# Kernel tuning notes

Hardware: AMD Instinct MI355X
Metric: run time of the kernel (lower is better)

The kernel has to match this reference:

```python
import jax, jax.numpy as jnp
import numpy as np

N, E, B = 20000, 320000, 64
NODE_DIM, EDGE_DIM, H, T = 64, 32, 128, 256
L = 5            # propagation_depth
DELTA = 1.0      # avg_d['log']
N_AGG, N_SCAL = 4, 3


def _w(k, shape):
    return jax.random.normal(k, shape, jnp.float32) / np.sqrt(shape[-2])


def setup_inputs() -> dict:
    key = jax.random.key(0)
    ks = jax.random.split(key, 12)
    return {
        "node_feat": jax.random.normal(ks[0], (N, NODE_DIM), jnp.float32),
        "edge_feat": jax.random.normal(ks[1], (E, EDGE_DIM), jnp.float32),
        "W_in": _w(ks[2], (NODE_DIM, H)),
        "b_in": jnp.zeros((H,), jnp.float32),
        "pre_W": _w(ks[3], (L, 2 * H + EDGE_DIM, H)),
        "pre_b": jnp.zeros((L, H), jnp.float32),
        "post_W": _w(ks[4], (L, H + N_AGG * N_SCAL * H, H)),
        "post_b": jnp.zeros((L, H), jnp.float32),
        "out_W1": _w(ks[5], (3 * H, H)),
        "out_b1": jnp.zeros((H,), jnp.float32),
        "out_W2": _w(ks[6], (H, T)),
        "out_b2": jnp.zeros((T,), jnp.float32),
        "src": jax.random.randint(ks[7], (E,), 0, N),
        "dst": jax.random.randint(ks[8], (E,), 0, N),
        "node2graph": jnp.sort(jax.random.randint(ks[9], (N,), 0, B)),
    }


def _forward(node_feat, edge_feat, W_in, b_in, pre_W, pre_b, post_W, post_b,
             out_W1, out_b1, out_W2, out_b2, src, dst, node2graph):
    # input node MLP (Linear + ReLU)
    h = jax.nn.relu(node_feat @ W_in + b_in)                       # [N, H]

    # degree-based scalers (constant across layers)
    deg = jax.ops.segment_sum(jnp.ones((E,), h.dtype), dst, num_segments=N)
    has_edge = (deg > 0)[:, None]
    inv_deg = jnp.where(deg > 0, 1.0 / jnp.maximum(deg, 1.0), 0.0)[:, None]
    logd = jnp.log(deg + 1.0)
    amp = (logd / DELTA)[:, None]                                  # amplification
    att = jnp.where(logd > 0, DELTA / jnp.maximum(logd, 1e-12), 1.0)[:, None]

    def step(h, p):
        pW, pb, qW, qb = p
        # pretrans on concat(src feat, dst feat, edge feat)
        m_in = jnp.concatenate([h[src], h[dst], edge_feat], axis=-1)  # [E, 2H+De]
        m = jax.nn.relu(m_in @ pW + pb)                               # [E, H]
        # multi-aggregator gather
        s = jax.ops.segment_sum(m, dst, num_segments=N)
        mean = s * inv_deg
        mx = jnp.where(has_edge, jax.ops.segment_max(m, dst, num_segments=N), 0.0)
        mn = jnp.where(has_edge, jax.ops.segment_min(m, dst, num_segments=N), 0.0)
        agg = jnp.concatenate([mean, mx, mn, s], axis=-1)             # [N, 4H]
        scaled = jnp.concatenate([agg, agg * amp, agg * att], axis=-1)  # [N, 12H]
        # posttrans on concat(h, aggregated)
        h_new = jax.nn.relu(jnp.concatenate([h, scaled], axis=-1) @ qW + qb)
        return h + h_new, None                                        # residual

    h, _ = jax.lax.scan(step, h, (pre_W, pre_b, post_W, post_b))

    # multi-aggregator readout over graphs
    g_sum = jax.ops.segment_sum(h, node2graph, num_segments=B)
    g_cnt = jax.ops.segment_sum(jnp.ones((N, 1), h.dtype), node2graph, num_segments=B)
    g_mean = g_sum / jnp.maximum(g_cnt, 1.0)
    g_max = jnp.where(g_cnt > 0, jax.ops.segment_max(h, node2graph, num_segments=B), 0.0)
    readout = jnp.concatenate([g_mean, g_max, g_sum], axis=-1)        # [B, 3H]
    return jax.nn.relu(readout @ out_W1 + out_b1) @ out_W2 + out_b2   # [B, T]


def reference(node_feat, edge_feat, W_in, b_in, pre_W, pre_b, post_W, post_b,
              out_W1, out_b1, out_W2, out_b2, src, dst, node2graph):
    return _forward(node_feat, edge_feat, W_in, b_in, pre_W, pre_b, post_W, post_b,
                    out_W1, out_b1, out_W2, out_b2, src, dst, node2graph)
```

## Files before the change

### kernel.cpp

```cpp
#include <hip/hip_runtime.h>

#define H 128
#define NODE_DIM 64
#define EDGE_DIM 32
#define KPRE (2*H + EDGE_DIM)
#define KPOST (13*H)
#define T_OUT 256
#define L_DEPTH 5
#define POST_FRAGS (52*8*64)
#define Y_FRAGS (4*16*64)
#define EF_FRAGS (8*64)
#define RCH 8

typedef short short8v __attribute__((ext_vector_type(8)));
typedef float float4v __attribute__((ext_vector_type(4)));

__device__ __forceinline__ unsigned short f2bf(float x) {
    unsigned int b = __float_as_uint(x);
    return (unsigned short)((b + 0x7fffu + ((b >> 16) & 1u)) >> 16);
}
__device__ __forceinline__ float bf2f(unsigned short u) {
    return __uint_as_float((unsigned int)u << 16);
}

__global__ void k_input_mlp(const float* __restrict__ nf, const float* __restrict__ W,
                            const float* __restrict__ b, float* __restrict__ h,
                            unsigned short* __restrict__ h_bf, int N) {
    int gid = blockIdx.x * blockDim.x + threadIdx.x;
    int n = gid >> 7, c = gid & 127;
    if (n >= N) return;
    const float* nrow = nf + (size_t)n * NODE_DIM;
    float acc = 0.f;
#pragma unroll 8
    for (int k = 0; k < NODE_DIM; ++k)
        acc += nrow[k] * W[k * H + c];
    acc += b[c];
    acc = fmaxf(acc, 0.f);
    h[(size_t)n * H + c] = acc;
    h_bf[(size_t)n * H + c] = f2bf(acc);
}

__global__ void k_hist(const int* __restrict__ dst, int* __restrict__ deg_i, int E) {
    int e = blockIdx.x * blockDim.x + threadIdx.x;
    if (e < E) atomicAdd(&deg_i[dst[e]], 1);
}

__global__ __launch_bounds__(1024) void k_scan(const int* __restrict__ deg_i,
                                               int* __restrict__ row_start,
                                               int* __restrict__ cursor, int N) {
    __shared__ int part[1024];
    int t = threadIdx.x;
    int per = (N + 1023) / 1024;
    int base = t * per;
    int s = 0;
    for (int i = 0; i < per; ++i) {
        int idx = base + i;
        if (idx < N) s += deg_i[idx];
    }
    part[t] = s;
    __syncthreads();
    for (int off = 1; off < 1024; off <<= 1) {
        int v = (t >= off) ? part[t - off] : 0;
        __syncthreads();
        part[t] += v;
        __syncthreads();
    }
    int run = (t == 0) ? 0 : part[t - 1];
    for (int i = 0; i < per; ++i) {
        int idx = base + i;
        if (idx < N) {
            row_start[idx] = run;
            cursor[idx] = run;
            run += deg_i[idx];
        }
    }
    if (t == 1023) row_start[N] = run;
}

__global__ void k_sortscatter(const int* __restrict__ src, const int* __restrict__ dst,
                              int* __restrict__ cursor, int* __restrict__ es_src,
                              int* __restrict__ es_eid, int E) {
    int e = blockIdx.x * blockDim.x + threadIdx.x;
    if (e >= E) return;
    int pos = atomicAdd(&cursor[dst[e]], 1);
    es_src[pos] = src[e];
    es_eid[pos] = e;
}

__global__ void k_efsort(const float* __restrict__ ef, const int* __restrict__ es_eid,
                         unsigned short* __restrict__ efs_bf, int E) {
    int t = blockIdx.x * 256 + threadIdx.x;
    int p = t >> 2, q = t & 3;
    if (p >= E) return;
    int eid = es_eid[p];
    const float* sp = ef + (size_t)eid * EDGE_DIM + q * 8;
    float4 v0 = *(const float4*)sp;
    float4 v1 = *(const float4*)(sp + 4);
    short8v o;
    o[0] = (short)f2bf(v0.x); o[1] = (short)f2bf(v0.y);
    o[2] = (short)f2bf(v0.z); o[3] = (short)f2bf(v0.w);
    o[4] = (short)f2bf(v1.x); o[5] = (short)f2bf(v1.y);
    o[6] = (short)f2bf(v1.z); o[7] = (short)f2bf(v1.w);
    *(short8v*)(efs_bf + (size_t)p * EDGE_DIM + q * 8) = o;
}

__global__ void k_scalers(const int* __restrict__ deg_i, float* __restrict__ invd,
                          float* __restrict__ amp, float* __restrict__ att, int N) {
    int n = blockIdx.x * blockDim.x + threadIdx.x;
    if (n >= N) return;
    float d = (float)deg_i[n];
    invd[n] = (d > 0.f) ? (1.f / d) : 0.f;
    float ld = logf(d + 1.f);
    amp[n] = ld;
    att[n] = (d > 0.f) ? (1.f / ld) : 1.f;
}

__global__ void k_gbounds(const int* __restrict__ n2g, int* __restrict__ g_start,
                          int N, int B) {
    int n = blockIdx.x * 256 + threadIdx.x;
    if (n > N) return;
    int cur = (n < N) ? n2g[n] : B;
    int prev = (n == 0) ? -1 : n2g[n - 1];
    for (int g = prev + 1; g <= cur && g <= B; ++g)
        g_start[g] = n;
}

__global__ void k_wconv_all(const float* __restrict__ pre_W,
                            const float* __restrict__ post_W,
                            short* __restrict__ wf_y_all,
                            short* __restrict__ wf_post_all,
                            short* __restrict__ wf_ef_all) {
    const int wrow[13] = {0, 256, 384, 512, 768, 896, 1024, 1280, 1408, 1536, 128, 640, 1152};
    int t = blockIdx.x * 256 + threadIdx.x;
    if (t < L_DEPTH * POST_FRAGS) {
        int l = t / POST_FRAGS, tt = t - l * POST_FRAGS;
        const float* qW = post_W + (size_t)l * KPOST * H;
        int lane = tt & 63, fc = tt >> 6;
        int b = fc >> 5, ks = (fc >> 3) & 3, cb = fc & 7;
        int col = cb * 16 + (lane & 15);
        int k0 = wrow[b] + ks * 32 + ((lane >> 4) << 3);
        short8v o;
#pragma unroll
        for (int j = 0; j < 8; ++j)
            o[j] = (short)f2bf(qW[(size_t)(k0 + j) * H + col]);
        *(short8v*)(wf_post_all + (size_t)t * 8) = o;
        return;
    }
    t -= L_DEPTH * POST_FRAGS;
    if (t < L_DEPTH * Y_FRAGS) {
        int l = t / Y_FRAGS, tt = t - l * Y_FRAGS;
        const float* pW = pre_W + (size_t)l * KPRE * H;
        int lane = tt & 63, fc = tt >> 6;
        int kglob = fc >> 4, cb = fc & 15;
        int col = cb * 16 + (lane & 15);
        int k0 = kglob * 32 + ((lane >> 4) << 3);
        int rowoff = (col < 128) ? 0 : 128;
        int c = col & 127;
        short8v o;
#pragma unroll
        for (int j = 0; j < 8; ++j)
            o[j] = (short)f2bf(pW[(size_t)(rowoff + k0 + j) * H + c]);
        *(short8v*)(wf_y_all + (size_t)t * 8) = o;
        return;
    }
    t -= L_DEPTH * Y_FRAGS;
    if (t >= L_DEPTH * EF_FRAGS) return;
    int l = t / EF_FRAGS, tt = t - l * EF_FRAGS;
    int lane = tt & 63, cb = tt >> 6;
    int col = cb * 16 + (lane & 15);
    int k0 = (lane >> 4) << 3;
    const float* pW = pre_W + (size_t)l * KPRE * H;
    short8v o;
#pragma unroll
    for (int j = 0; j < 8; ++j)
        o[j] = (short)f2bf(pW[(size_t)(2 * H + k0 + j) * H + col]);
    *(short8v*)(wf_ef_all + (size_t)t * 8) = o;
}

__global__ __launch_bounds__(256) void k_ygemm_mfma(
    const unsigned short* __restrict__ h_bf, const short* __restrict__ Wf,
    unsigned short* __restrict__ Y1bf, unsigned short* __restrict__ Y2bf, int N)
{
    __shared__ __align__(16) short Xs[64 * 128];
    int tid = threadIdx.x;
    int n0 = blockIdx.x * 64;
    int lane = tid & 63, wave = tid >> 6;
    float4v acc[16];
#pragma unroll
    for (int cb = 0; cb < 16; ++cb) acc[cb] = (float4v){0.f, 0.f, 0.f, 0.f};

    int rs = tid >> 4, c0 = (tid & 15) * 8;
#pragma unroll
    for (int j = 0; j < 4; ++j) {
        int r = rs + j * 16;
        int n = n0 + r;
        uint4 v = make_uint4(0, 0, 0, 0);
        if (n < N) v = *(const uint4*)(h_bf + (size_t)n * H + c0);
        *(uint4*)((char*)Xs + r * 256 + ((c0 * 2) ^ ((r & 7) << 4))) = v;
    }
    __syncthreads();
    int rloc = wave * 16 + (lane & 15);
    int swz = (rloc & 7) << 4;
#pragma unroll
    for (int ks = 0; ks < 4; ++ks) {
        int boff = rloc * 256 + (((ks * 64) + ((lane >> 4) << 4)) ^ swz);
        short8v a = *(short8v*)((char*)Xs + boff);
        const short* wp = Wf + ((size_t)(ks * 16) * 64 + lane) * 8;
#pragma unroll
        for (int cb = 0; cb < 16; ++cb) {
            short8v b = *(const short8v*)(wp + (size_t)cb * 512);
            acc[cb] = __builtin_amdgcn_mfma_f32_16x16x32_bf16(a, b, acc[cb], 0, 0, 0);
        }
    }
    int col0 = lane & 15;
    int row0 = wave * 16 + ((lane >> 4) << 2);
#pragma unroll
    for (int cb = 0; cb < 16; ++cb) {
        int col = cb * 16 + col0;
#pragma unroll
        for (int r = 0; r < 4; ++r) {
            int n = n0 + row0 + r;
            if (n < N) {
                if (col < 128) Y1bf[(size_t)n * H + col] = f2bf(acc[cb][r]);
                else           Y2bf[(size_t)n * H + (col - 128)] = f2bf(acc[cb][r]);
            }
        }
    }
}

__global__ __launch_bounds__(256) void k_efw(
    const unsigned short* __restrict__ efs_bf, const short* __restrict__ WfEf,
    unsigned short* __restrict__ EFW, int E)
{
    __shared__ __align__(16) unsigned short buf[4][16][128];
    int tid = threadIdx.x, lane = tid & 63, w = tid >> 6;
    int p0 = blockIdx.x * 256 + w * 64;
    short8v bfr[8];
#pragma unroll
    for (int cb = 0; cb < 8; ++cb)
        bfr[cb] = *(const short8v*)(WfEf + (size_t)(cb * 64 + lane) * 8);
#pragma unroll
    for (int t4 = 0; t4 < 4; ++t4) {
        int rowb = p0 + t4 * 16;
        int ar = rowb + (lane & 15);
        short8v a = {};
        if (ar < E)
            a = *(const short8v*)(efs_bf + (size_t)ar * EDGE_DIM + ((lane >> 4) << 3));
        float4v acc[8];
#pragma unroll
        for (int cb = 0; cb < 8; ++cb)
            acc[cb] = __builtin_amdgcn_mfma_f32_16x16x32_bf16(
                a, bfr[cb], (float4v){0.f, 0.f, 0.f, 0.f}, 0, 0, 0);
#pragma unroll
        for (int cb = 0; cb < 8; ++cb)
#pragma unroll
            for (int r = 0; r < 4; ++r)
                buf[w][((lane >> 4) << 2) + r][cb * 16 + (lane & 15)] = f2bf(acc[cb][r]);
#pragma unroll
        for (int j = 0; j < 4; ++j) {
            int lr = (lane >> 4) + j * 4;
            int gr = rowb + lr;
            uint4 v = *(const uint4*)&buf[w][lr][(lane & 15) * 8];
            if (gr < E)
                *(uint4*)(EFW + (size_t)gr * H + (lane & 15) * 8) = v;
        }
    }
}

__global__ __launch_bounds__(256) void k_edge_agg(
    const unsigned short* __restrict__ Y1bf, const unsigned short* __restrict__ Y2bf,
    const unsigned short* __restrict__ EFW, const float* __restrict__ pb,
    const int* __restrict__ es_src, const int* __restrict__ row_start,
    unsigned short* __restrict__ s_out, unsigned short* __restrict__ mx_out,
    unsigned short* __restrict__ mn_out, int N)
{
    __shared__ float red[4][3][128];
    int n = blockIdx.x;
    int tid = threadIdx.x, lane = tid & 63, w = tid >> 6;
    int start = row_start[n], end = row_start[n + 1];
    int cnt = end - start;
    int per = (cnt + 3) >> 2;
    int p0 = start + w * per;
    int p1 = min(p0 + per, end);
    unsigned int y2u = *(const unsigned int*)(Y2bf + (size_t)n * H + 2 * lane);
    float2 pbv = *(const float2*)(pb + 2 * lane);
    float y20 = bf2f((unsigned short)(y2u & 0xffffu)) + pbv.x;
    float y21 = bf2f((unsigned short)(y2u >> 16)) + pbv.y;
    float s0 = 0.f, s1 = 0.f;
    float mx0 = -3.4e38f, mx1 = -3.4e38f, mn0 = 3.4e38f, mn1 = 3.4e38f;
#pragma unroll 2
    for (int p = p0; p < p1; ++p) {
        int sn = __builtin_amdgcn_readfirstlane(es_src[p]);
        unsigned int y1u = *(const unsigned int*)(Y1bf + (size_t)sn * H + 2 * lane);
        unsigned int eu  = *(const unsigned int*)(EFW + (size_t)p * H + 2 * lane);
        float m0 = fmaxf(bf2f((unsigned short)(y1u & 0xffffu)) +
                         bf2f((unsigned short)(eu & 0xffffu)) + y20, 0.f);
        float m1 = fmaxf(bf2f((unsigned short)(y1u >> 16)) +
                         bf2f((unsigned short)(eu >> 16)) + y21, 0.f);
        s0 += m0; s1 += m1;
        mx0 = fmaxf(mx0, m0); mx1 = fmaxf(mx1, m1);
        mn0 = fminf(mn0, m0); mn1 = fminf(mn1, m1);
    }
    red[w][0][2 * lane] = s0;  red[w][0][2 * lane + 1] = s1;
    red[w][1][2 * lane] = mx0; red[w][1][2 * lane + 1] = mx1;
    red[w][2][2 * lane] = mn0; red[w][2][2 * lane + 1] = mn1;
    __syncthreads();
    if (tid < 128) {
        int c = tid;
        float s  = (red[0][0][c] + red[1][0][c]) + (red[2][0][c] + red[3][0][c]);
        float mx = fmaxf(fmaxf(red[0][1][c], red[1][1][c]),
                         fmaxf(red[2][1][c], red[3][1][c]));
        float mn = fminf(fminf(red[0][2][c], red[1][2][c]),
                         fminf(red[2][2][c], red[3][2][c]));
        if (cnt == 0) { s = 0.f; mx = 0.f; mn = 0.f; }
        size_t o = (size_t)n * H + c;
        s_out[o] = f2bf(s); mx_out[o] = f2bf(mx); mn_out[o] = f2bf(mn);
    }
}

__global__ __launch_bounds__(256) void k_post_mfma(
    float* __restrict__ h, unsigned short* __restrict__ h_bf,
    const unsigned short* __restrict__ s_in, const unsigned short* __restrict__ mx_in,
    const unsigned short* __restrict__ mn_in,
    const float* __restrict__ invd, const float* __restrict__ amp,
    const float* __restrict__ att,
    const short* __restrict__ Wf, const float* __restrict__ qb,
    const short* __restrict__ WfY, unsigned short* __restrict__ Y1bf,
    unsigned short* __restrict__ Y2bf, int doY, int N)
{
    __shared__ __align__(16) short Xs[32 * 128];
    int tid = threadIdx.x, lane = tid & 63, wave = tid >> 6;
    int rh = wave & 1, ch = wave >> 1;
    int n0 = blockIdx.x * 32;

    const unsigned short* const srcs[13] = {h_bf, mx_in, mn_in, s_in, mx_in, mn_in, s_in,
                                            mx_in, mn_in, s_in, s_in, s_in, s_in};
    const int grp_of[13] = {0, 0, 0, 0, 1, 1, 1, 2, 2, 2, 3, 4, 5};

    float4v acc[6][4];
#pragma unroll
    for (int g = 0; g < 6; ++g)
#pragma unroll
        for (int cb = 0; cb < 4; ++cb) acc[g][cb] = (float4v){0.f, 0.f, 0.f, 0.f};

    int arow = n0 + rh * 16 + (lane & 15);
    bool aok = arow < N;
    size_t abase = (size_t)arow * H + ((lane >> 4) << 3);

#pragma unroll
    for (int b = 0; b < 13; ++b) {
        const unsigned short* sp = srcs[b];
#pragma unroll
        for (int ks = 0; ks < 4; ++ks) {
            short8v a = {};
            if (aok) a = *(const short8v*)(sp + abase + ks * 32);
#pragma unroll
            for (int cb = 0; cb < 4; ++cb) {
                short8v bfrag = *(const short8v*)(
                    Wf + ((size_t)((b * 4 + ks) * 8 + ch * 4 + cb) * 64 + lane) * 8);
                acc[grp_of[b]][cb] =
                    __builtin_amdgcn_mfma_f32_16x16x32_bf16(a, bfrag, acc[grp_of[b]][cb], 0, 0, 0);
            }
        }
    }

    int col0 = lane & 15;
    int row0 = rh * 16 + ((lane >> 4) << 2);
    float s_invd[4], s_amp[4], s_att[4];
#pragma unroll
    for (int r = 0; r < 4; ++r) {
        int n = n0 + row0 + r;
        bool ok = n < N;
        s_invd[r] = ok ? invd[n] : 0.f;
        s_amp[r]  = ok ? amp[n]  : 0.f;
        s_att[r]  = ok ? att[n]  : 0.f;
    }
#pragma unroll
    for (int cb = 0; cb < 4; ++cb) {
        int col = (ch * 4 + cb) * 16 + col0;
        float bb = qb[col];
#pragma unroll
        for (int r = 0; r < 4; ++r) {
            int n = n0 + row0 + r;
            if (n < N) {
                float v = acc[0][cb][r]
                        + s_amp[r] * acc[1][cb][r] + s_att[r] * acc[2][cb][r]
                        + s_invd[r] * (acc[3][cb][r] + s_amp[r] * acc[4][cb][r]
                                       + s_att[r] * acc[5][cb][r]);
                size_t o = (size_t)n * H + col;
                float nv = h[o] + fmaxf(v + bb, 0.f);
                h[o] = nv;
                unsigned short us = f2bf(nv);
                h_bf[o] = us;
                if (doY) {
                    int rr = row0 + r;
                    *(short*)((char*)Xs + rr * 256 + ((col * 2) ^ ((rr & 7) << 4))) = (short)us;
                }
            }
        }
    }
    if (doY) {
        __syncthreads();
        float4v yacc[8];
#pragma unroll
        for (int i = 0; i < 8; ++i) yacc[i] = (float4v){0.f, 0.f, 0.f, 0.f};
#pragma unroll
        for (int t16 = 0; t16 < 2; ++t16) {
            int rloc = t16 * 16 + (lane & 15);
            int swz = (rloc & 7) << 4;
#pragma unroll
            for (int ks = 0; ks < 4; ++ks) {
                int boff = rloc * 256 + (((ks * 64) + ((lane >> 4) << 4)) ^ swz);
                short8v a = *(short8v*)((char*)Xs + boff);
#pragma unroll
                for (int cb = 0; cb < 4; ++cb) {
                    const short* wp = WfY + ((size_t)(ks * 16 + wave * 4 + cb) * 64 + lane) * 8;
                    short8v b = *(const short8v*)wp;
                    yacc[t16 * 4 + cb] =
                        __builtin_amdgcn_mfma_f32_16x16x32_bf16(a, b, yacc[t16 * 4 + cb], 0, 0, 0);
                }
            }
        }
#pragma unroll
        for (int t16 = 0; t16 < 2; ++t16) {
#pragma unroll
            for (int cb = 0; cb < 4; ++cb) {
                int col = (wave * 4 + cb) * 16 + col0;
                int r0 = t16 * 16 + ((lane >> 4) << 2);
#pragma unroll
                for (int r = 0; r < 4; ++r) {
                    int n = n0 + r0 + r;
                    if (n < N) {
                        unsigned short v = f2bf(yacc[t16 * 4 + cb][r]);
                        if (col < 128) Y1bf[(size_t)n * H + col] = v;
                        else           Y2bf[(size_t)n * H + (col - 128)] = v;
                    }
                }
            }
        }
    }
}

__global__ __launch_bounds__(256) void k_readout_part(
    const float* __restrict__ h, const int* __restrict__ g_start,
    float* __restrict__ psum, float* __restrict__ pmax, int B)
{
    __shared__ float rs[2][128], rm[2][128];
    int blk = blockIdx.x;
    int b = blk / RCH, chunk = blk % RCH;
    int tid = threadIdx.x;
    int c = tid & 127, half = tid >> 7;
    int g0 = g_start[b], g1 = g_start[b + 1];
    int cnt = g1 - g0;
    int per = (cnt + RCH - 1) / RCH;
    int n0 = g0 + chunk * per;
    int n1 = min(n0 + per, g1);
    float s = 0.f, m = -3.4e38f;
    for (int n = n0 + half; n < n1; n += 2) {
        float v = h[(size_t)n * H + c];
        s += v;
        m = fmaxf(m, v);
    }
    rs[half][c] = s;
    rm[half][c] = m;
    __syncthreads();
    if (tid < 128) {
        size_t o = ((size_t)b * RCH + chunk) * H + c;
        psum[o] = rs[0][c] + rs[1][c];
        pmax[o] = fmaxf(rm[0][c], rm[1][c]);
    }
}

__global__ __launch_bounds__(256) void k_readout_final2(
    const float* __restrict__ psum, const float* __restrict__ pmax,
    const int* __restrict__ g_start,
    const float* __restrict__ W1, const float* __restrict__ b1,
    const float* __restrict__ W2, const float* __restrict__ b2,
    float* __restrict__ out)
{
    __shared__ float xv[3 * H];
    __shared__ float hid[H];
    int b = blockIdx.x, tid = threadIdx.x;
    int cnt = g_start[b + 1] - g_start[b];
    if (tid < 128) {
        int c = tid;
        float s = 0.f, m = -3.4e38f;
#pragma unroll
        for (int j = 0; j < RCH; ++j) {
            size_t o = ((size_t)b * RCH + j) * H + c;
            s += psum[o];
            m = fmaxf(m, pmax[o]);
        }
        float rc = 1.f / fmaxf((float)cnt, 1.f);
        xv[c]         = s * rc;
        xv[H + c]     = (cnt > 0) ? m : 0.f;
        xv[2 * H + c] = s;
    }
    __syncthreads();
    if (tid < 128) {
        float acc = 0.f;
        for (int k = 0; k < 3 * H; ++k)
            acc += xv[k] * W1[k * H + tid];
        hid[tid] = fmaxf(acc + b1[tid], 0.f);
    }
    __syncthreads();
    float acc = 0.f;
#pragma unroll 8
    for (int k = 0; k < H; ++k)
        acc += hid[k] * W2[k * T_OUT + tid];
    out[(size_t)b * T_OUT + tid] = acc + b2[tid];
}

extern "C" void kernel_launch(void* const* d_in, const int* in_sizes, int n_in,
                              void* d_out, int out_size, void* d_ws, size_t ws_size,
                              hipStream_t stream) {
    const float* node_feat = (const float*)d_in[0];
    const float* edge_feat = (const float*)d_in[1];
    const float* W_in  = (const float*)d_in[2];
    const float* b_in  = (const float*)d_in[3];
    const float* pre_W = (const float*)d_in[4];
    const float* pre_b = (const float*)d_in[5];
    const float* post_W = (const float*)d_in[6];
    const float* post_b = (const float*)d_in[7];
    const float* out_W1 = (const float*)d_in[8];
    const float* out_b1 = (const float*)d_in[9];
    const float* out_W2 = (const float*)d_in[10];
    const float* out_b2 = (const float*)d_in[11];
    const int* src = (const int*)d_in[12];
    const int* dst = (const int*)d_in[13];
    const int* n2g = (const int*)d_in[14];

    int N = in_sizes[0] / NODE_DIM;
    int E = in_sizes[1] / EDGE_DIM;
    int B = out_size / T_OUT;
    float* out = (float*)d_out;

    float* ws = (float*)d_ws;
    float* h    = ws; ws += (size_t)N * H;
    float* invd = ws; ws += N;
    float* amp  = ws; ws += N;
    float* att  = ws; ws += N;
    float* psum = ws; ws += (size_t)B * RCH * H;
    float* pmax = ws; ws += (size_t)B * RCH * H;
    ws = (float*)(((uintptr_t)ws + 15) & ~(uintptr_t)15);
    unsigned short* h_bf  = (unsigned short*)ws;
    unsigned short* s_buf = h_bf  + (size_t)N * H;
    unsigned short* mx    = s_buf + (size_t)N * H;
    unsigned short* mn    = mx    + (size_t)N * H;
    unsigned short* Y1bf  = mn    + (size_t)N * H;
    unsigned short* Y2bf  = Y1bf  + (size_t)N * H;
    unsigned short* efs_bf = Y2bf + (size_t)N * H;
    unsigned short* EFW    = efs_bf + (size_t)E * EDGE_DIM;
    short* wf_post_all = (short*)(EFW + (size_t)E * H);
    short* wf_y_all    = wf_post_all + (size_t)L_DEPTH * POST_FRAGS * 8;
    short* wf_ef_all   = wf_y_all + (size_t)L_DEPTH * Y_FRAGS * 8;
    int* deg_i     = (int*)(wf_ef_all + (size_t)L_DEPTH * EF_FRAGS * 8);
    int* row_start = deg_i + N;
    int* cursor    = row_start + N + 1;
    int* es_src    = cursor + N;
    int* es_eid    = es_src + E;
    int* g_start   = es_eid + E;

    k_input_mlp<<<((size_t)N * H + 255) / 256, 256, 0, stream>>>(node_feat, W_in, b_in,
                                                                 h, h_bf, N);

    hipMemsetAsync(deg_i, 0, (size_t)N * sizeof(int), stream);
    k_hist<<<(E + 255) / 256, 256, 0, stream>>>(dst, deg_i, E);
    k_scan<<<1, 1024, 0, stream>>>(deg_i, row_start, cursor, N);
    k_sortscatter<<<(E + 255) / 256, 256, 0, stream>>>(src, dst, cursor, es_src, es_eid, E);
    k_efsort<<<((size_t)E * 4 + 255) / 256, 256, 0, stream>>>(edge_feat, es_eid, efs_bf, E);
    k_scalers<<<(N + 255) / 256, 256, 0, stream>>>(deg_i, invd, amp, att, N);
    k_gbounds<<<(N + 256) / 256, 256, 0, stream>>>(n2g, g_start, N, B);

    {
        int tot = L_DEPTH * (POST_FRAGS + Y_FRAGS + EF_FRAGS);
        k_wconv_all<<<(tot + 255) / 256, 256, 0, stream>>>(pre_W, post_W, wf_y_all,
                                                           wf_post_all, wf_ef_all);
    }

    k_ygemm_mfma<<<(N + 63) / 64, 256, 0, stream>>>(h_bf, wf_y_all, Y1bf, Y2bf, N);

    for (int l = 0; l < L_DEPTH; ++l) {
        k_efw<<<(E + 255) / 256, 256, 0, stream>>>(
            efs_bf, wf_ef_all + (size_t)l * EF_FRAGS * 8, EFW, E);
        k_edge_agg<<<N, 256, 0, stream>>>(
            Y1bf, Y2bf, EFW, pre_b + (size_t)l * H,
            es_src, row_start, s_buf, mx, mn, N);
        int doY = (l < L_DEPTH - 1) ? 1 : 0;
        k_post_mfma<<<(N + 31) / 32, 256, 0, stream>>>(
            h, h_bf, s_buf, mx, mn, invd, amp, att,
            wf_post_all + (size_t)l * POST_FRAGS * 8, post_b + (size_t)l * H,
            doY ? (wf_y_all + (size_t)(l + 1) * Y_FRAGS * 8) : wf_y_all,
            Y1bf, Y2bf, doY, N);
    }

    k_readout_part<<<B * RCH, 256, 0, stream>>>(h, g_start, psum, pmax, B);
    k_readout_final2<<<B, 256, 0, stream>>>(psum, pmax, g_start,
                                            out_W1, out_b1, out_W2, out_b2, out);
}
```

Baseline: 715.3 us.

## Map one wave per node in edge aggregation and halve post-MFMA row tile

The edge aggregation kernel now assigns one wavefront per destination node, four nodes per block, instead of splitting each node's edges across four waves. This removes the shared-memory reduction and block barrier, and writes outputs as packed 32-bit stores. The post-transform MFMA kernel now uses 16-row tiles with each wave owning 32 output columns, which doubles the block count to raise occupancy but re-reads the weight fragments more often. The per-node work is now serialized within one wave, so high-degree nodes take longer.

```diff
diff --git a/kernel.cpp b/kernel.cpp
--- a/kernel.cpp
+++ b/kernel.cpp
@@ -274,22 +274,20 @@
     unsigned short* __restrict__ s_out, unsigned short* __restrict__ mx_out,
     unsigned short* __restrict__ mn_out, int N)
 {
-    __shared__ float red[4][3][128];
-    int n = blockIdx.x;
     int tid = threadIdx.x, lane = tid & 63, w = tid >> 6;
+    int n = blockIdx.x * 4 + w;
+    if (n >= N) return;
     int start = row_start[n], end = row_start[n + 1];
-    int cnt = end - start;
-    int per = (cnt + 3) >> 2;
-    int p0 = start + w * per;
-    int p1 = min(p0 + per, end);
+    bool any = end > start;
     unsigned int y2u = *(const unsigned int*)(Y2bf + (size_t)n * H + 2 * lane);
     float2 pbv = *(const float2*)(pb + 2 * lane);
     float y20 = bf2f((unsigned short)(y2u & 0xffffu)) + pbv.x;
     float y21 = bf2f((unsigned short)(y2u >> 16)) + pbv.y;
     float s0 = 0.f, s1 = 0.f;
-    float mx0 = -3.4e38f, mx1 = -3.4e38f, mn0 = 3.4e38f, mn1 = 3.4e38f;
+    float mx0 = any ? -3.4e38f : 0.f, mx1 = any ? -3.4e38f : 0.f;
+    float mn0 = any ? 3.4e38f : 0.f,  mn1 = any ? 3.4e38f : 0.f;
 #pragma unroll 2
-    for (int p = p0; p < p1; ++p) {
+    for (int p = start; p < end; ++p) {
         int sn = __builtin_amdgcn_readfirstlane(es_src[p]);
         unsigned int y1u = *(const unsigned int*)(Y1bf + (size_t)sn * H + 2 * lane);
         unsigned int eu  = *(const unsigned int*)(EFW + (size_t)p * H + 2 * lane);
@@ -301,21 +299,10 @@
         mx0 = fmaxf(mx0, m0); mx1 = fmaxf(mx1, m1);
         mn0 = fminf(mn0, m0); mn1 = fminf(mn1, m1);
     }
-    red[w][0][2 * lane] = s0;  red[w][0][2 * lane + 1] = s1;
-    red[w][1][2 * lane] = mx0; red[w][1][2 * lane + 1] = mx1;
-    red[w][2][2 * lane] = mn0; red[w][2][2 * lane + 1] = mn1;
-    __syncthreads();
-    if (tid < 128) {
-        int c = tid;
-        float s  = (red[0][0][c] + red[1][0][c]) + (red[2][0][c] + red[3][0][c]);
-        float mx = fmaxf(fmaxf(red[0][1][c], red[1][1][c]),
-                         fmaxf(red[2][1][c], red[3][1][c]));
-        float mn = fminf(fminf(red[0][2][c], red[1][2][c]),
-                         fminf(red[2][2][c], red[3][2][c]));
-        if (cnt == 0) { s = 0.f; mx = 0.f; mn = 0.f; }
-        size_t o = (size_t)n * H + c;
-        s_out[o] = f2bf(s); mx_out[o] = f2bf(mx); mn_out[o] = f2bf(mn);
-    }
+    size_t o = (size_t)n * H + 2 * lane;
+    *(unsigned int*)(s_out + o)  = (unsigned int)f2bf(s0)  | ((unsigned int)f2bf(s1)  << 16);
+    *(unsigned int*)(mx_out + o) = (unsigned int)f2bf(mx0) | ((unsigned int)f2bf(mx1) << 16);
+    *(unsigned int*)(mn_out + o) = (unsigned int)f2bf(mn0) | ((unsigned int)f2bf(mn1) << 16);
 }
 
 __global__ __launch_bounds__(256) void k_post_mfma(
@@ -328,22 +315,21 @@
     const short* __restrict__ WfY, unsigned short* __restrict__ Y1bf,
     unsigned short* __restrict__ Y2bf, int doY, int N)
 {
-    __shared__ __align__(16) short Xs[32 * 128];
-    int tid = threadIdx.x, lane = tid & 63, wave = tid >> 6;
-    int rh = wave & 1, ch = wave >> 1;
-    int n0 = blockIdx.x * 32;
+    __shared__ __align__(16) short Xs[16 * 128];
+    int tid = threadIdx.x, lane = tid & 63, ch = tid >> 6;
+    int n0 = blockIdx.x * 16;
 
     const unsigned short* const srcs[13] = {h_bf, mx_in, mn_in, s_in, mx_in, mn_in, s_in,
                                             mx_in, mn_in, s_in, s_in, s_in, s_in};
     const int grp_of[13] = {0, 0, 0, 0, 1, 1, 1, 2, 2, 2, 3, 4, 5};
 
-    float4v acc[6][4];
+    float4v acc[6][2];
 #pragma unroll
     for (int g = 0; g < 6; ++g)
 #pragma unroll
-        for (int cb = 0; cb < 4; ++cb) acc[g][cb] = (float4v){0.f, 0.f, 0.f, 0.f};
-
-    int arow = n0 + rh * 16 + (lane & 15);
+        for (int cb = 0; cb < 2; ++cb) acc[g][cb] = (float4v){0.f, 0.f, 0.f, 0.f};
+
+    int arow = n0 + (lane & 15);
     bool aok = arow < N;
     size_t abase = (size_t)arow * H + ((lane >> 4) << 3);
 
@@ -355,9 +341,9 @@
             short8v a = {};
             if (aok) a = *(const short8v*)(sp + abase + ks * 32);
 #pragma unroll
-            for (int cb = 0; cb < 4; ++cb) {
+            for (int cb = 0; cb < 2; ++cb) {
                 short8v bfrag = *(const short8v*)(
-                    Wf + ((size_t)((b * 4 + ks) * 8 + ch * 4 + cb) * 64 + lane) * 8);
+                    Wf + ((size_t)((b * 4 + ks) * 8 + ch * 2 + cb) * 64 + lane) * 8);
                 acc[grp_of[b]][cb] =
                     __builtin_amdgcn_mfma_f32_16x16x32_bf16(a, bfrag, acc[grp_of[b]][cb], 0, 0, 0);
             }
@@ -365,7 +351,7 @@
     }
 
     int col0 = lane & 15;
-    int row0 = rh * 16 + ((lane >> 4) << 2);
+    int row0 = (lane >> 4) << 2;
     float s_invd[4], s_amp[4], s_att[4];
 #pragma unroll
     for (int r = 0; r < 4; ++r) {
@@ -376,8 +362,8 @@
         s_att[r]  = ok ? att[n]  : 0.f;
     }
 #pragma unroll
-    for (int cb = 0; cb < 4; ++cb) {
-        int col = (ch * 4 + cb) * 16 + col0;
+    for (int cb = 0; cb < 2; ++cb) {
+        int col = (ch * 2 + cb) * 16 + col0;
         float bb = qb[col];
 #pragma unroll
         for (int r = 0; r < 4; ++r) {
@@ -401,40 +387,32 @@
     }
     if (doY) {
         __syncthreads();
-        float4v yacc[8];
-#pragma unroll
-        for (int i = 0; i < 8; ++i) yacc[i] = (float4v){0.f, 0.f, 0.f, 0.f};
-#pragma unroll
-        for (int t16 = 0; t16 < 2; ++t16) {
-            int rloc = t16 * 16 + (lane & 15);
-            int swz = (rloc & 7) << 4;
-#pragma unroll
-            for (int ks = 0; ks < 4; ++ks) {
-                int boff = rloc * 256 + (((ks * 64) + ((lane >> 4) << 4)) ^ swz);
-                short8v a = *(short8v*)((char*)Xs + boff);
-#pragma unroll
-                for (int cb = 0; cb < 4; ++cb) {
-                    const short* wp = WfY + ((size_t)(ks * 16 + wave * 4 + cb) * 64 + lane) * 8;
-                    short8v b = *(const short8v*)wp;
-                    yacc[t16 * 4 + cb] =
-                        __builtin_amdgcn_mfma_f32_16x16x32_bf16(a, b, yacc[t16 * 4 + cb], 0, 0, 0);
-                }
+        float4v yacc[4];
+#pragma unroll
+        for (int i = 0; i < 4; ++i) yacc[i] = (float4v){0.f, 0.f, 0.f, 0.f};
+        int rloc = lane & 15;
+        int swz = (rloc & 7) << 4;
+#pragma unroll
+        for (int ks = 0; ks < 4; ++ks) {
+            int boff = rloc * 256 + (((ks * 64) + ((lane >> 4) << 4)) ^ swz);
+            short8v a = *(short8v*)((char*)Xs + boff);
+#pragma unroll
+            for (int cb = 0; cb < 4; ++cb) {
+                const short* wp = WfY + ((size_t)(ks * 16 + ch * 4 + cb) * 64 + lane) * 8;
+                short8v b = *(const short8v*)wp;
+                yacc[cb] = __builtin_amdgcn_mfma_f32_16x16x32_bf16(a, b, yacc[cb], 0, 0, 0);
             }
         }
 #pragma unroll
-        for (int t16 = 0; t16 < 2; ++t16) {
-#pragma unroll
-            for (int cb = 0; cb < 4; ++cb) {
-                int col = (wave * 4 + cb) * 16 + col0;
-                int r0 = t16 * 16 + ((lane >> 4) << 2);
-#pragma unroll
-                for (int r = 0; r < 4; ++r) {
-                    int n = n0 + r0 + r;
-                    if (n < N) {
-                        unsigned short v = f2bf(yacc[t16 * 4 + cb][r]);
-                        if (col < 128) Y1bf[(size_t)n * H + col] = v;
-                        else           Y2bf[(size_t)n * H + (col - 128)] = v;
-                    }
+        for (int cb = 0; cb < 4; ++cb) {
+            int col = (ch * 4 + cb) * 16 + col0;
+#pragma unroll
+            for (int r = 0; r < 4; ++r) {
+                int n = n0 + row0 + r;
+                if (n < N) {
+                    unsigned short v = f2bf(yacc[cb][r]);
+                    if (col < 128) Y1bf[(size_t)n * H + col] = v;
+                    else           Y2bf[(size_t)n * H + (col - 128)] = v;
                 }
             }
         }
@@ -583,11 +561,11 @@
     for (int l = 0; l < L_DEPTH; ++l) {
         k_efw<<<(E + 255) / 256, 256, 0, stream>>>(
             efs_bf, wf_ef_all + (size_t)l * EF_FRAGS * 8, EFW, E);
-        k_edge_agg<<<N, 256, 0, stream>>>(
+        k_edge_agg<<<(N + 3) / 4, 256, 0, stream>>>(
             Y1bf, Y2bf, EFW, pre_b + (size_t)l * H,
             es_src, row_start, s_buf, mx, mn, N);
         int doY = (l < L_DEPTH - 1) ? 1 : 0;
-        k_post_mfma<<<(N + 31) / 32, 256, 0, stream>>>(
+        k_post_mfma<<<(N + 15) / 16, 256, 0, stream>>>(
             h, h_bf, s_buf, mx, mn, invd, amp, att,
             wf_post_all + (size_t)l * POST_FRAGS * 8, post_b + (size_t)l * H,
             doY ? (wf_y_all + (size_t)(l + 1) * Y_FRAGS * 8) : wf_y_all,
```

New measurement: 803.0 us. 12.3% more time.

## Map one wave per node in edge aggregation and dedupe A-loads in post GEMM

Applied to the files above, without the earlier changes.

The edge aggregation kernel now assigns each destination node to a single wavefront (four nodes per block) instead of splitting a node's edges across four waves. This removes the shared-memory reduction and block barrier, and lets each lane write packed bf16 pairs. The post GEMM is restructured so each distinct A source (h, max, min, sum) is loaded once per k-step and reused across all weight blocks that consume it, instead of reloading the same aggregate for every scaler group. The trade-off is less parallelism per node, so high-degree nodes become serial within one wave.

```diff
diff --git a/kernel.cpp b/kernel.cpp
--- a/kernel.cpp
+++ b/kernel.cpp
@@ -274,22 +274,20 @@
     unsigned short* __restrict__ s_out, unsigned short* __restrict__ mx_out,
     unsigned short* __restrict__ mn_out, int N)
 {
-    __shared__ float red[4][3][128];
-    int n = blockIdx.x;
     int tid = threadIdx.x, lane = tid & 63, w = tid >> 6;
+    int n = blockIdx.x * 4 + w;
+    if (n >= N) return;
     int start = row_start[n], end = row_start[n + 1];
-    int cnt = end - start;
-    int per = (cnt + 3) >> 2;
-    int p0 = start + w * per;
-    int p1 = min(p0 + per, end);
+    bool any = end > start;
     unsigned int y2u = *(const unsigned int*)(Y2bf + (size_t)n * H + 2 * lane);
     float2 pbv = *(const float2*)(pb + 2 * lane);
     float y20 = bf2f((unsigned short)(y2u & 0xffffu)) + pbv.x;
     float y21 = bf2f((unsigned short)(y2u >> 16)) + pbv.y;
     float s0 = 0.f, s1 = 0.f;
-    float mx0 = -3.4e38f, mx1 = -3.4e38f, mn0 = 3.4e38f, mn1 = 3.4e38f;
+    float mx0 = any ? -3.4e38f : 0.f, mx1 = any ? -3.4e38f : 0.f;
+    float mn0 = any ? 3.4e38f : 0.f,  mn1 = any ? 3.4e38f : 0.f;
 #pragma unroll 2
-    for (int p = p0; p < p1; ++p) {
+    for (int p = start; p < end; ++p) {
         int sn = __builtin_amdgcn_readfirstlane(es_src[p]);
         unsigned int y1u = *(const unsigned int*)(Y1bf + (size_t)sn * H + 2 * lane);
         unsigned int eu  = *(const unsigned int*)(EFW + (size_t)p * H + 2 * lane);
@@ -301,22 +299,20 @@
         mx0 = fmaxf(mx0, m0); mx1 = fmaxf(mx1, m1);
         mn0 = fminf(mn0, m0); mn1 = fminf(mn1, m1);
     }
-    red[w][0][2 * lane] = s0;  red[w][0][2 * lane + 1] = s1;
-    red[w][1][2 * lane] = mx0; red[w][1][2 * lane + 1] = mx1;
-    red[w][2][2 * lane] = mn0; red[w][2][2 * lane + 1] = mn1;
-    __syncthreads();
-    if (tid < 128) {
-        int c = tid;
-        float s  = (red[0][0][c] + red[1][0][c]) + (red[2][0][c] + red[3][0][c]);
-        float mx = fmaxf(fmaxf(red[0][1][c], red[1][1][c]),
-                         fmaxf(red[2][1][c], red[3][1][c]));
-        float mn = fminf(fminf(red[0][2][c], red[1][2][c]),
-                         fminf(red[2][2][c], red[3][2][c]));
-        if (cnt == 0) { s = 0.f; mx = 0.f; mn = 0.f; }
-        size_t o = (size_t)n * H + c;
-        s_out[o] = f2bf(s); mx_out[o] = f2bf(mx); mn_out[o] = f2bf(mn);
-    }
-}
+    size_t o = (size_t)n * H + 2 * lane;
+    *(unsigned int*)(s_out + o)  = (unsigned int)f2bf(s0)  | ((unsigned int)f2bf(s1)  << 16);
+    *(unsigned int*)(mx_out + o) = (unsigned int)f2bf(mx0) | ((unsigned int)f2bf(mx1) << 16);
+    *(unsigned int*)(mn_out + o) = (unsigned int)f2bf(mn0) | ((unsigned int)f2bf(mn1) << 16);
+}
+
+#define POST_MM(b, g)                                                               \
+    _Pragma("unroll")                                                               \
+    for (int cb = 0; cb < 4; ++cb) {                                                \
+        short8v bfrag = *(const short8v*)(                                          \
+            Wf + ((size_t)(((b) * 4 + ks) * 8 + ch * 4 + cb) * 64 + lane) * 8);     \
+        acc[g][cb] = __builtin_amdgcn_mfma_f32_16x16x32_bf16(a, bfrag, acc[g][cb],  \
+                                                             0, 0, 0);              \
+    }
 
 __global__ __launch_bounds__(256) void k_post_mfma(
     float* __restrict__ h, unsigned short* __restrict__ h_bf,
@@ -333,10 +329,6 @@
     int rh = wave & 1, ch = wave >> 1;
     int n0 = blockIdx.x * 32;
 
-    const unsigned short* const srcs[13] = {h_bf, mx_in, mn_in, s_in, mx_in, mn_in, s_in,
-                                            mx_in, mn_in, s_in, s_in, s_in, s_in};
-    const int grp_of[13] = {0, 0, 0, 0, 1, 1, 1, 2, 2, 2, 3, 4, 5};
-
     float4v acc[6][4];
 #pragma unroll
     for (int g = 0; g < 6; ++g)
@@ -348,20 +340,37 @@
     size_t abase = (size_t)arow * H + ((lane >> 4) << 3);
 
 #pragma unroll
-    for (int b = 0; b < 13; ++b) {
-        const unsigned short* sp = srcs[b];
-#pragma unroll
-        for (int ks = 0; ks < 4; ++ks) {
-            short8v a = {};
-            if (aok) a = *(const short8v*)(sp + abase + ks * 32);
-#pragma unroll
-            for (int cb = 0; cb < 4; ++cb) {
-                short8v bfrag = *(const short8v*)(
-                    Wf + ((size_t)((b * 4 + ks) * 8 + ch * 4 + cb) * 64 + lane) * 8);
-                acc[grp_of[b]][cb] =
-                    __builtin_amdgcn_mfma_f32_16x16x32_bf16(a, bfrag, acc[grp_of[b]][cb], 0, 0, 0);
-            }
-        }
+    for (int ks = 0; ks < 4; ++ks) {
+        short8v a = {};
+        if (aok) a = *(const short8v*)(h_bf + abase + ks * 32);
+        POST_MM(0, 0)
+    }
+#pragma unroll
+    for (int ks = 0; ks < 4; ++ks) {
+        short8v a = {};
+        if (aok) a = *(const short8v*)(mx_in + abase + ks * 32);
+        POST_MM(1, 0)
+        POST_MM(4, 1)
+        POST_MM(7, 2)
+    }
+#pragma unroll
+    for (int ks = 0; ks < 4; ++ks) {
+        short8v a = {};
+        if (aok) a = *(const short8v*)(mn_in + abase + ks * 32);
+        POST_MM(2, 0)
+        POST_MM(5, 1)
+        POST_MM(8, 2)
+    }
+#pragma unroll
+    for (int ks = 0; ks < 4; ++ks) {
+        short8v a = {};
+        if (aok) a = *(const short8v*)(s_in + abase + ks * 32);
+        POST_MM(3, 0)
+        POST_MM(6, 1)
+        POST_MM(9, 2)
+        POST_MM(10, 3)
+        POST_MM(11, 4)
+        POST_MM(12, 5)
     }
 
     int col0 = lane & 15;
@@ -583,7 +592,7 @@
     for (int l = 0; l < L_DEPTH; ++l) {
         k_efw<<<(E + 255) / 256, 256, 0, stream>>>(
             efs_bf, wf_ef_all + (size_t)l * EF_FRAGS * 8, EFW, E);
-        k_edge_agg<<<N, 256, 0, stream>>>(
+        k_edge_agg<<<(N + 3) / 4, 256, 0, stream>>>(
             Y1bf, Y2bf, EFW, pre_b + (size_t)l * H,
             es_src, row_start, s_buf, mx, mn, N);
         int doY = (l < L_DEPTH - 1) ? 1 : 0;
```

Measured after the change: 837.4 us. 1.17x slower.

## Fuse edge-feature GEMM into Y and post kernels; one wave per node in edge_agg

Applied to the files above, without the earlier changes.

The per-layer edge-feature projection is merged into the preceding Y-GEMM or post-transform launch as extra blocks, so it runs alongside that work and the separate per-layer launch goes away. The edge aggregation kernel now gives each node a single wave instead of splitting its edges across four waves. This drops the shared-memory cross-wave reduction and barrier, and the outputs are written as packed bf16 pairs. In exchange, a high-degree node is handled serially by one wave, and the fused kernels reserve extra LDS, which may lower occupancy for the post GEMM blocks.

```diff
diff --git a/kernel.cpp b/kernel.cpp
--- a/kernel.cpp
+++ b/kernel.cpp
@@ -177,64 +177,13 @@
     *(short8v*)(wf_ef_all + (size_t)t * 8) = o;
 }
 
-__global__ __launch_bounds__(256) void k_ygemm_mfma(
-    const unsigned short* __restrict__ h_bf, const short* __restrict__ Wf,
-    unsigned short* __restrict__ Y1bf, unsigned short* __restrict__ Y2bf, int N)
+__device__ __forceinline__ void efw_body(
+    int blk, const unsigned short* __restrict__ efs_bf,
+    const short* __restrict__ WfEf, unsigned short* __restrict__ EFW, int E,
+    unsigned short (*buf)[16][128])
 {
-    __shared__ __align__(16) short Xs[64 * 128];
-    int tid = threadIdx.x;
-    int n0 = blockIdx.x * 64;
-    int lane = tid & 63, wave = tid >> 6;
-    float4v acc[16];
-#pragma unroll
-    for (int cb = 0; cb < 16; ++cb) acc[cb] = (float4v){0.f, 0.f, 0.f, 0.f};
-
-    int rs = tid >> 4, c0 = (tid & 15) * 8;
-#pragma unroll
-    for (int j = 0; j < 4; ++j) {
-        int r = rs + j * 16;
-        int n = n0 + r;
-        uint4 v = make_uint4(0, 0, 0, 0);
-        if (n < N) v = *(const uint4*)(h_bf + (size_t)n * H + c0);
-        *(uint4*)((char*)Xs + r * 256 + ((c0 * 2) ^ ((r & 7) << 4))) = v;
-    }
-    __syncthreads();
-    int rloc = wave * 16 + (lane & 15);
-    int swz = (rloc & 7) << 4;
-#pragma unroll
-    for (int ks = 0; ks < 4; ++ks) {
-        int boff = rloc * 256 + (((ks * 64) + ((lane >> 4) << 4)) ^ swz);
-        short8v a = *(short8v*)((char*)Xs + boff);
-        const short* wp = Wf + ((size_t)(ks * 16) * 64 + lane) * 8;
-#pragma unroll
-        for (int cb = 0; cb < 16; ++cb) {
-            short8v b = *(const short8v*)(wp + (size_t)cb * 512);
-            acc[cb] = __builtin_amdgcn_mfma_f32_16x16x32_bf16(a, b, acc[cb], 0, 0, 0);
-        }
-    }
-    int col0 = lane & 15;
-    int row0 = wave * 16 + ((lane >> 4) << 2);
-#pragma unroll
-    for (int cb = 0; cb < 16; ++cb) {
-        int col = cb * 16 + col0;
-#pragma unroll
-        for (int r = 0; r < 4; ++r) {
-            int n = n0 + row0 + r;
-            if (n < N) {
-                if (col < 128) Y1bf[(size_t)n * H + col] = f2bf(acc[cb][r]);
-                else           Y2bf[(size_t)n * H + (col - 128)] = f2bf(acc[cb][r]);
-            }
-        }
-    }
-}
-
-__global__ __launch_bounds__(256) void k_efw(
-    const unsigned short* __restrict__ efs_bf, const short* __restrict__ WfEf,
-    unsigned short* __restrict__ EFW, int E)
-{
-    __shared__ __align__(16) unsigned short buf[4][16][128];
     int tid = threadIdx.x, lane = tid & 63, w = tid >> 6;
-    int p0 = blockIdx.x * 256 + w * 64;
+    int p0 = blk * 256 + w * 64;
     short8v bfr[8];
 #pragma unroll
     for (int cb = 0; cb < 8; ++cb)
@@ -267,6 +216,64 @@
     }
 }
 
+__global__ __launch_bounds__(256) void k_y0_fat(
+    const unsigned short* __restrict__ h_bf, const short* __restrict__ Wf,
+    unsigned short* __restrict__ Y1bf, unsigned short* __restrict__ Y2bf, int N,
+    const unsigned short* __restrict__ efs_bf, const short* __restrict__ WfEf,
+    unsigned short* __restrict__ EFW, int E, int nYBlocks)
+{
+    __shared__ __align__(16) short Xs[64 * 128];
+    __shared__ __align__(16) unsigned short buf[4][16][128];
+    if (blockIdx.x >= nYBlocks) {
+        efw_body(blockIdx.x - nYBlocks, efs_bf, WfEf, EFW, E, buf);
+        return;
+    }
+    int tid = threadIdx.x;
+    int n0 = blockIdx.x * 64;
+    int lane = tid & 63, wave = tid >> 6;
+    float4v acc[16];
+#pragma unroll
+    for (int cb = 0; cb < 16; ++cb) acc[cb] = (float4v){0.f, 0.f, 0.f, 0.f};
+
+    int rs = tid >> 4, c0 = (tid & 15) * 8;
+#pragma unroll
+    for (int j = 0; j < 4; ++j) {
+        int r = rs + j * 16;
+        int n = n0 + r;
+        uint4 v = make_uint4(0, 0, 0, 0);
+        if (n < N) v = *(const uint4*)(h_bf + (size_t)n * H + c0);
+        *(uint4*)((char*)Xs + r * 256 + ((c0 * 2) ^ ((r & 7) << 4))) = v;
+    }
+    __syncthreads();
+    int rloc = wave * 16 + (lane & 15);
+    int swz = (rloc & 7) << 4;
+#pragma unroll
+    for (int ks = 0; ks < 4; ++ks) {
+        int boff = rloc * 256 + (((ks * 64) + ((lane >> 4) << 4)) ^ swz);
+        short8v a = *(short8v*)((char*)Xs + boff);
+        const short* wp = Wf + ((size_t)(ks * 16) * 64 + lane) * 8;
+#pragma unroll
+        for (int cb = 0; cb < 16; ++cb) {
+            short8v b = *(const short8v*)(wp + (size_t)cb * 512);
+            acc[cb] = __builtin_amdgcn_mfma_f32_16x16x32_bf16(a, b, acc[cb], 0, 0, 0);
+        }
+    }
+    int col0 = lane & 15;
+    int row0 = wave * 16 + ((lane >> 4) << 2);
+#pragma unroll
+    for (int cb = 0; cb < 16; ++cb) {
+        int col = cb * 16 + col0;
+#pragma unroll
+        for (int r = 0; r < 4; ++r) {
+            int n = n0 + row0 + r;
+            if (n < N) {
+                if (col < 128) Y1bf[(size_t)n * H + col] = f2bf(acc[cb][r]);
+                else           Y2bf[(size_t)n * H + (col - 128)] = f2bf(acc[cb][r]);
+            }
+        }
+    }
+}
+
 __global__ __launch_bounds__(256) void k_edge_agg(
     const unsigned short* __restrict__ Y1bf, const unsigned short* __restrict__ Y2bf,
     const unsigned short* __restrict__ EFW, const float* __restrict__ pb,
@@ -274,22 +281,20 @@
     unsigned short* __restrict__ s_out, unsigned short* __restrict__ mx_out,
     unsigned short* __restrict__ mn_out, int N)
 {
-    __shared__ float red[4][3][128];
-    int n = blockIdx.x;
     int tid = threadIdx.x, lane = tid & 63, w = tid >> 6;
+    int n = blockIdx.x * 4 + w;
+    if (n >= N) return;
     int start = row_start[n], end = row_start[n + 1];
-    int cnt = end - start;
-    int per = (cnt + 3) >> 2;
-    int p0 = start + w * per;
-    int p1 = min(p0 + per, end);
+    bool any = end > start;
     unsigned int y2u = *(const unsigned int*)(Y2bf + (size_t)n * H + 2 * lane);
     float2 pbv = *(const float2*)(pb + 2 * lane);
     float y20 = bf2f((unsigned short)(y2u & 0xffffu)) + pbv.x;
     float y21 = bf2f((unsigned short)(y2u >> 16)) + pbv.y;
     float s0 = 0.f, s1 = 0.f;
-    float mx0 = -3.4e38f, mx1 = -3.4e38f, mn0 = 3.4e38f, mn1 = 3.4e38f;
+    float mx0 = any ? -3.4e38f : 0.f, mx1 = any ? -3.4e38f : 0.f;
+    float mn0 = any ? 3.4e38f : 0.f,  mn1 = any ? 3.4e38f : 0.f;
 #pragma unroll 2
-    for (int p = p0; p < p1; ++p) {
+    for (int p = start; p < end; ++p) {
         int sn = __builtin_amdgcn_readfirstlane(es_src[p]);
         unsigned int y1u = *(const unsigned int*)(Y1bf + (size_t)sn * H + 2 * lane);
         unsigned int eu  = *(const unsigned int*)(EFW + (size_t)p * H + 2 * lane);
@@ -301,24 +306,13 @@
         mx0 = fmaxf(mx0, m0); mx1 = fmaxf(mx1, m1);
         mn0 = fminf(mn0, m0); mn1 = fminf(mn1, m1);
     }
-    red[w][0][2 * lane] = s0;  red[w][0][2 * lane + 1] = s1;
-    red[w][1][2 * lane] = mx0; red[w][1][2 * lane + 1] = mx1;
-    red[w][2][2 * lane] = mn0; red[w][2][2 * lane + 1] = mn1;
-    __syncthreads();
-    if (tid < 128) {
-        int c = tid;
-        float s  = (red[0][0][c] + red[1][0][c]) + (red[2][0][c] + red[3][0][c]);
-        float mx = fmaxf(fmaxf(red[0][1][c], red[1][1][c]),
-                         fmaxf(red[2][1][c], red[3][1][c]));
-        float mn = fminf(fminf(red[0][2][c], red[1][2][c]),
-                         fminf(red[2][2][c], red[3][2][c]));
-        if (cnt == 0) { s = 0.f; mx = 0.f; mn = 0.f; }
-        size_t o = (size_t)n * H + c;
-        s_out[o] = f2bf(s); mx_out[o] = f2bf(mx); mn_out[o] = f2bf(mn);
-    }
-}
-
-__global__ __launch_bounds__(256) void k_post_mfma(
+    size_t o = (size_t)n * H + 2 * lane;
+    *(unsigned int*)(s_out + o)  = (unsigned int)f2bf(s0)  | ((unsigned int)f2bf(s1)  << 16);
+    *(unsigned int*)(mx_out + o) = (unsigned int)f2bf(mx0) | ((unsigned int)f2bf(mx1) << 16);
+    *(unsigned int*)(mn_out + o) = (unsigned int)f2bf(mn0) | ((unsigned int)f2bf(mn1) << 16);
+}
+
+__global__ __launch_bounds__(256) void k_post_fat(
     float* __restrict__ h, unsigned short* __restrict__ h_bf,
     const unsigned short* __restrict__ s_in, const unsigned short* __restrict__ mx_in,
     const unsigned short* __restrict__ mn_in,
@@ -326,9 +320,16 @@
     const float* __restrict__ att,
     const short* __restrict__ Wf, const float* __restrict__ qb,
     const short* __restrict__ WfY, unsigned short* __restrict__ Y1bf,
-    unsigned short* __restrict__ Y2bf, int doY, int N)
+    unsigned short* __restrict__ Y2bf, int doY, int N,
+    const unsigned short* __restrict__ efs_bf, const short* __restrict__ WfEf,
+    unsigned short* __restrict__ EFW, int E, int nPostBlocks)
 {
     __shared__ __align__(16) short Xs[32 * 128];
+    __shared__ __align__(16) unsigned short buf[4][16][128];
+    if (blockIdx.x >= nPostBlocks) {
+        efw_body(blockIdx.x - nPostBlocks, efs_bf, WfEf, EFW, E, buf);
+        return;
+    }
     int tid = threadIdx.x, lane = tid & 63, wave = tid >> 6;
     int rh = wave & 1, ch = wave >> 1;
     int n0 = blockIdx.x * 32;
@@ -561,6 +562,10 @@
     int* es_eid    = es_src + E;
     int* g_start   = es_eid + E;
 
+    int nPostBlocks = (N + 31) / 32;
+    int nEfBlocks   = (E + 255) / 256;
+    int nYBlocks    = (N + 63) / 64;
+
     k_input_mlp<<<((size_t)N * H + 255) / 256, 256, 0, stream>>>(node_feat, W_in, b_in,
                                                                  h, h_bf, N);
 
@@ -578,20 +583,22 @@
                                                            wf_post_all, wf_ef_all);
     }
 
-    k_ygemm_mfma<<<(N + 63) / 64, 256, 0, stream>>>(h_bf, wf_y_all, Y1bf, Y2bf, N);
+    k_y0_fat<<<nYBlocks + nEfBlocks, 256, 0, stream>>>(
+        h_bf, wf_y_all, Y1bf, Y2bf, N, efs_bf, wf_ef_all, EFW, E, nYBlocks);
 
     for (int l = 0; l < L_DEPTH; ++l) {
-        k_efw<<<(E + 255) / 256, 256, 0, stream>>>(
-            efs_bf, wf_ef_all + (size_t)l * EF_FRAGS * 8, EFW, E);
-        k_edge_agg<<<N, 256, 0, stream>>>(
+        k_edge_agg<<<(N + 3) / 4, 256, 0, stream>>>(
             Y1bf, Y2bf, EFW, pre_b + (size_t)l * H,
             es_src, row_start, s_buf, mx, mn, N);
         int doY = (l < L_DEPTH - 1) ? 1 : 0;
-        k_post_mfma<<<(N + 31) / 32, 256, 0, stream>>>(
+        int grid = nPostBlocks + (doY ? nEfBlocks : 0);
+        k_post_fat<<<grid, 256, 0, stream>>>(
             h, h_bf, s_buf, mx, mn, invd, amp, att,
             wf_post_all + (size_t)l * POST_FRAGS * 8, post_b + (size_t)l * H,
             doY ? (wf_y_all + (size_t)(l + 1) * Y_FRAGS * 8) : wf_y_all,
-            Y1bf, Y2bf, doY, N);
+            Y1bf, Y2bf, doY, N,
+            efs_bf, doY ? (wf_ef_all + (size_t)(l + 1) * EF_FRAGS * 8) : wf_ef_all,
+            EFW, E, nPostBlocks);
     }
 
     k_readout_part<<<B * RCH, 256, 0, stream>>>(h, g_start, psum, pmax, B);
```

Measured after the change: 647.7 us, median of 2. 9.4% less time.
